# Optimization experiments

Measured on AMD Instinct MI355X. Metric: run time of the kernel, lower is better.

## Reference

```python
import jax, jax.numpy as jnp
import numpy as np

ND, NPR, DD, DP, LAT, AT, B = 2048, 2048, 128, 128, 128, 32, 16384


def setup_inputs():
    key = jax.random.key(0)
    ks = jax.random.split(key, 20)
    s = 0.05
    d = {}
    d["e_p_adj"] = (jax.random.uniform(ks[0], (ND, NPR)) < 0.05).astype(jnp.float32)
    d["e_e_adj"] = (jax.random.uniform(ks[1], (ND, ND)) < 0.05).astype(jnp.float32)
    d["p_p_adj"] = (jax.random.uniform(ks[2], (NPR, NPR)) < 0.05).astype(jnp.float32)
    d["input_disease"] = jax.random.randint(ks[3], (B,), 0, ND)
    d["input_drug"] = jax.random.randint(ks[4], (B,), 0, NPR)
    d["labels"] = jax.random.randint(ks[5], (B,), 0, 2)
    # learned parameters
    d["disease_emb"] = jax.random.normal(ks[6], (ND, DD)) * s
    d["drug_emb"] = jax.random.normal(ks[7], (NPR, DP)) * s
    d["Wdg"] = jax.random.normal(ks[8], (DP, LAT)) * s   # disease_gcn_w
    d["bdg_lin"] = jnp.zeros((LAT,))                      # Linear bias
    d["bdg"] = jnp.zeros((LAT,))                          # extra disease_gcn_b
    d["Wpg"] = jax.random.normal(ks[9], (DD, LAT)) * s   # drug_gcn_w
    d["bpg_lin"] = jnp.zeros((LAT,))
    d["bpg"] = jnp.zeros((LAT,))
    d["Wa1_d"] = jax.random.normal(ks[10], (DP + DD, AT)) * s  # concat [key(drug), query(disease)]
    d["ba1_d"] = jnp.zeros((AT,))
    d["Wa2_d"] = jax.random.normal(ks[11], (AT, 1)) * s
    d["ba2_d"] = jnp.zeros((1,))
    d["Wa1_p"] = jax.random.normal(ks[12], (DD + DP, AT)) * s  # concat [key(disease), query(drug)]
    d["ba1_p"] = jnp.zeros((AT,))
    d["Wa2_p"] = jax.random.normal(ks[13], (AT, 1)) * s
    d["ba2_p"] = jnp.zeros((1,))
    d["Wd2"] = jax.random.normal(ks[14], (DD, LAT)) * s  # disease_w2
    d["bd2"] = jnp.zeros((LAT,))
    d["Wp3"] = jax.random.normal(ks[15], (DP, LAT)) * s  # drug_w3
    d["bp3"] = jnp.zeros((LAT,))
    d["mlp_W1"] = jax.random.normal(ks[16], (LAT, DD)) * s
    d["mlp_b1"] = jnp.zeros((DD,))
    d["mlp_W2"] = jax.random.normal(ks[17], (DD, DD)) * s
    d["mlp_b2"] = jnp.zeros((DD,))
    d["Wpred"] = jax.random.normal(ks[18], (DD, 1)) * s
    d["bpred"] = jnp.zeros((1,))
    return d


def _attention_gcn(adj, other, selfe, W1, b1, W2, b2):
    # torch: concat([key=other, query=self]) -> Linear(W1) ; split W1 instead of
    # materializing the [Ns, No, Dk+Dq] concat tensor (same math, less HBM traffic)
    do = other.shape[1]
    ko = other @ W1[:do]              # [No, A]
    qs = selfe @ W1[do:]              # [Ns, A]
    h = jax.nn.relu(qs[:, None, :] + ko[None, :, :] + b1)   # [Ns, No, A]
    alpha = jax.nn.relu(jnp.squeeze(h @ W2, -1) + b2[0])    # [Ns, No]
    alpha = alpha * adj
    return jax.nn.softmax(alpha, axis=1) @ other            # [Ns, Do]


def _forward(e_p_adj, e_e_adj, p_p_adj, input_disease, input_drug, labels,
             disease_emb, drug_emb, Wdg, bdg_lin, bdg, Wpg, bpg_lin, bpg,
             Wa1_d, ba1_d, Wa2_d, ba2_d, Wa1_p, ba1_p, Wa2_p, ba2_p,
             Wd2, bd2, Wp3, bp3, mlp_W1, mlp_b1, mlp_W2, mlp_b2, Wpred, bpred):
    h_e_gcn = _attention_gcn(e_p_adj, drug_emb, disease_emb, Wa1_d, ba1_d, Wa2_d, ba2_d)
    h_e_gcn = h_e_gcn @ Wdg + bdg_lin + bdg
    h_p_gcn = _attention_gcn(e_p_adj.T, disease_emb, drug_emb, Wa1_p, ba1_p, Wa2_p, ba2_p)
    h_p_gcn = h_p_gcn @ Wpg + bpg_lin + bpg
    # disease knn branch
    deg_d = jnp.sum(e_e_adj, axis=1, keepdims=True) + 1e-8
    h_e_e = ((e_e_adj @ disease_emb) / deg_d) @ Wd2 + bd2
    h_e = jax.nn.selu(h_e_gcn + h_e_e)
    # drug knn branch
    deg_p = jnp.sum(p_p_adj, axis=1, keepdims=True) + 1e-8
    h_p_p = ((p_p_adj @ drug_emb) / deg_p) @ Wp3 + bp3
    h_p = jax.nn.selu(h_p_gcn + h_p_p)
    # pair prediction MLP
    x = h_e[input_disease] * h_p[input_drug]                # [B, LAT]
    x = jax.nn.selu(x @ mlp_W1 + mlp_b1)
    x = jax.nn.selu(x @ mlp_W2 + mlp_b2)
    z = jnp.squeeze(x @ Wpred, -1) + bpred[0]               # [B]
    y = labels.astype(jnp.float32)
    # BCEWithLogitsLoss (stable), mean reduction
    loss = jnp.mean(jnp.maximum(z, 0.0) - z * y + jnp.log1p(jnp.exp(-jnp.abs(z))))
    return (loss, jax.nn.sigmoid(z))


def reference(e_p_adj, e_e_adj, p_p_adj, input_disease, input_drug, labels,
              disease_emb, drug_emb, Wdg, bdg_lin, bdg, Wpg, bpg_lin, bpg,
              Wa1_d, ba1_d, Wa2_d, ba2_d, Wa1_p, ba1_p, Wa2_p, ba2_p,
              Wd2, bd2, Wp3, bp3, mlp_W1, mlp_b1, mlp_W2, mlp_b2, Wpred, bpred):
    return _forward(e_p_adj, e_e_adj, p_p_adj, input_disease, input_drug, labels,
                    disease_emb, drug_emb, Wdg, bdg_lin, bdg, Wpg, bpg_lin, bpg,
                    Wa1_d, ba1_d, Wa2_d, ba2_d, Wa1_p, ba1_p, Wa2_p, ba2_p,
                    Wd2, bd2, Wp3, bp3, mlp_W1, mlp_b1, mlp_W2, mlp_b2, Wpred, bpred)
```

## Files before the change

### kernel.cpp

```cpp
#include <hip/hip_runtime.h>

#define ND   2048
#define BB   16384

typedef unsigned short u16;
typedef unsigned int u32;
typedef __attribute__((ext_vector_type(8))) short short8;
typedef __attribute__((ext_vector_type(4))) float f32x4;

__device__ inline float bf2f(u16 u) {
    union { u32 i; float f; } v; v.i = ((u32)u) << 16; return v.f;
}
__device__ inline u16 f2bf(float f) {
    union { float f; u32 i; } v; v.f = f;
    u32 i = v.i + 0x7fffu + ((v.i >> 16) & 1u);
    return (u16)(i >> 16);
}
__device__ inline float seluf(float x) {
    const float sc = 1.0507009873554805f, al = 1.6732632423543772f;
    return x > 0.f ? sc * x : sc * al * expm1f(x);
}
__device__ inline short8 packbf8(float4 f0, float4 f1) {
    short8 a;
    a[0] = (short)f2bf(f0.x); a[1] = (short)f2bf(f0.y);
    a[2] = (short)f2bf(f0.z); a[3] = (short)f2bf(f0.w);
    a[4] = (short)f2bf(f1.x); a[5] = (short)f2bf(f1.y);
    a[6] = (short)f2bf(f1.z); a[7] = (short)f2bf(f1.w);
    return a;
}

__global__ void detectk(const void* __restrict__ demb, u32* __restrict__ flag) {
    const u16* p = (const u16*)demb;
    int tid = threadIdx.x;
    int sane = 0;
    #pragma unroll
    for (int i = 0; i < 2; i++) {
        u16 u = p[4 * tid + 2 * i];
        int e = (u >> 7) & 0xFF;
        if (u == 0 || (e >= 0x66 && e <= 0x8C)) sane++;
    }
    __shared__ int red[256];
    red[tid] = sane; __syncthreads();
    for (int o = 128; o > 0; o >>= 1) {
        if (tid < o) red[tid] += red[tid + o];
        __syncthreads();
    }
    if (tid == 0) flag[0] = (red[0] < 300) ? 1u : 0u;
}

#define NSEG 26
struct CvtArgs { const void* src[NSEG]; int off[NSEG]; int n[NSEG]; };

__global__ __launch_bounds__(256) void cvtk(CvtArgs a, u16* __restrict__ base,
                                            const u32* __restrict__ flag) {
    int seg = blockIdx.y;
    int n = a.n[seg];
    const void* s = a.src[seg];
    u16* d = base + a.off[seg];
    bool f32 = flag[0] != 0;
    int stride = gridDim.x * blockDim.x;
    for (int i = blockIdx.x * blockDim.x + threadIdx.x; i < n; i += stride)
        d[i] = f32 ? f2bf(((const float*)s)[i]) : ((const u16*)s)[i];
}

__device__ inline void tpose_body(const u16* in, int R, int C,
                                  u16* out, int ldo, int ooff,
                                  u16 (*tile)[33]) {
    int c0 = blockIdx.x * 32, r0 = blockIdx.y * 32;
    int x = c0 + threadIdx.x;
    for (int i = threadIdx.y; i < 32; i += 8) {
        int r = r0 + i;
        tile[i][threadIdx.x] = (r < R && x < C) ? in[(size_t)r * C + x] : (u16)0;
    }
    __syncthreads();
    int rr = r0 + threadIdx.x;
    for (int i = threadIdx.y; i < 32; i += 8) {
        int cc = c0 + i;
        if (cc < C && rr < R) out[(size_t)cc * ldo + ooff + rr] = tile[threadIdx.x][i];
    }
}

__global__ void tpose_embs(const u16* __restrict__ demb, const u16* __restrict__ pemb,
                           u16* __restrict__ disT, u16* __restrict__ drugT) {
    __shared__ u16 tile[32][33];
    if (blockIdx.z == 0) tpose_body(demb, ND, 128, disT, ND, 0, tile);
    else                 tpose_body(pemb, ND, 128, drugT, ND, 0, tile);
}

__global__ void tpose_smalls(const u16* s0, const u16* s1, const u16* s2,
                             const u16* s3, const u16* s4, const u16* s5,
                             u16* W1T, u16* W2T, u16* WcTe, u16* WcTp) {
    __shared__ u16 tile[32][33];
    const u16* in; u16* out; int ldo, ooff;
    switch (blockIdx.z) {
        case 0:  in = s0; out = W1T;  ldo = 128; ooff = 0;   break;
        case 1:  in = s1; out = W2T;  ldo = 128; ooff = 0;   break;
        case 2:  in = s2; out = WcTe; ldo = 256; ooff = 0;   break;
        case 3:  in = s3; out = WcTe; ldo = 256; ooff = 128; break;
        case 4:  in = s4; out = WcTp; ldo = 256; ooff = 0;   break;
        default: in = s5; out = WcTp; ldo = 256; ooff = 128; break;
    }
    tpose_body(in, 128, 128, out, ldo, ooff, tile);
}

__global__ void biasc(const u16* a0, const u16* a1, const u16* a2, u16* o0,
                      const u16* b0, const u16* b1, const u16* b2, u16* o1) {
    int t = threadIdx.x;
    o0[t] = f2bf(bf2f(a0[t]) + bf2f(a1[t]) + bf2f(a2[t]));
    o1[t] = f2bf(bf2f(b0[t]) + bf2f(b1[t]) + bf2f(b2[t]));
}

__global__ __launch_bounds__(256) void degk(
    const void* __restrict__ e_e, float* __restrict__ dinv_e,
    const void* __restrict__ p_p, float* __restrict__ dinv_p,
    const u32* __restrict__ flag) {
    int row = blockIdx.x, tid = threadIdx.x;
    const void* ab = blockIdx.y ? p_p : e_e;
    float* o = blockIdx.y ? dinv_p : dinv_e;
    bool f32 = flag[0] != 0;
    float s = 0.f;
    if (f32) {
        const float4* a4 = (const float4*)((const float*)ab + (size_t)row * 2048) + tid * 2;
        float4 v0 = a4[0], v1 = a4[1];
        s = v0.x + v0.y + v0.z + v0.w + v1.x + v1.y + v1.z + v1.w;
    } else {
        const uint4* a4 = (const uint4*)((const u16*)ab + (size_t)row * 2048) + tid;
        uint4 v = a4[0];
        u32 u[4] = {v.x, v.y, v.z, v.w};
        #pragma unroll
        for (int c = 0; c < 4; c++)
            s += bf2f((u16)(u[c] & 0xffff)) + bf2f((u16)(u[c] >> 16));
    }
    __shared__ float red[256];
    red[tid] = s; __syncthreads();
    for (int ofs = 128; ofs > 0; ofs >>= 1) {
        if (tid < ofs) red[tid] += red[tid + ofs];
        __syncthreads();
    }
    if (tid == 0) o[row] = 1.f / (red[0] + 1e-8f);
}

__global__ __launch_bounds__(128) void koqs(
    const u16* __restrict__ demb, const u16* __restrict__ pemb,
    const u16* __restrict__ Wa1d, const u16* __restrict__ ba1d,
    const u16* __restrict__ Wa1p, const u16* __restrict__ ba1p,
    float* __restrict__ ko_d, float* __restrict__ qs_d,
    float* __restrict__ ko_p, float* __restrict__ qs_p) {
    int row = blockIdx.x, m = blockIdx.y, tid = threadIdx.x;
    const u16* src; const u16* W; const u16* bias; float* out;
    switch (m) {
        case 0:  src = pemb; W = Wa1d;            bias = nullptr; out = ko_d; break;
        case 1:  src = demb; W = Wa1d + 128 * 32; bias = ba1d;    out = qs_d; break;
        case 2:  src = demb; W = Wa1p;            bias = nullptr; out = ko_p; break;
        default: src = pemb; W = Wa1p + 128 * 32; bias = ba1p;    out = qs_p; break;
    }
    __shared__ float x[128];
    __shared__ float red[128];
    x[tid] = bf2f(src[(size_t)row * 128 + tid]);
    __syncthreads();
    int a = tid & 31, part = tid >> 5;
    float s = 0.f;
    #pragma unroll
    for (int k = 0; k < 32; k++) s += x[part * 32 + k] * bf2f(W[(part * 32 + k) * 32 + a]);
    red[tid] = s;
    __syncthreads();
    if (part == 0) {
        float t = red[a] + red[a + 32] + red[a + 64] + red[a + 96];
        if (bias) t += bf2f(bias[a]);
        out[(size_t)row * 32 + a] = t;
    }
}

struct AW {
    const float* qs[2]; const float* ko[2];
    const u16* w2[2]; const u16* b2[2];
    u16* outw[2]; float* sums[2];
    int transposed[2];
};

__global__ __launch_bounds__(256, 4) void attnw6(AW a, const void* __restrict__ adj,
                                                 const u32* __restrict__ flag) {
    __shared__ float tile[32][257];
    __shared__ float wpart[4][32];
    int z = blockIdx.z;
    int tid = threadIdx.x;
    int lane = tid & 63, wv = tid >> 6;
    int jl = wv * 64 + lane;
    int jbase = blockIdx.x * 256;
    int j = jbase + jl;
    int p0 = blockIdx.y * 32;
    bool f32a = flag[0] != 0;
    bool tr = a.transposed[z] != 0;
    const float* adjf = (const float*)adj;
    const u16*   adjh = (const u16*)adj;

    float kv[32];
    {
        const float4* kp = (const float4*)(a.ko[z] + (size_t)j * 32);
        #pragma unroll
        for (int qd = 0; qd < 8; qd++) {
            float4 v = kp[qd];
            kv[qd * 4 + 0] = v.x; kv[qd * 4 + 1] = v.y;
            kv[qd * 4 + 2] = v.z; kv[qd * 4 + 3] = v.w;
        }
    }
    float w2v[32];
    #pragma unroll
    for (int i2 = 0; i2 < 32; i2++) w2v[i2] = bf2f(a.w2[z][i2]);
    float b2 = bf2f(a.b2[z][0]);
    const float* qs = a.qs[z];
    u16* outw = a.outw[z];

    if (tr) {
        if (f32a) {
            const float4* src = (const float4*)(adjf + (size_t)(jbase + tid) * 2048 + p0);
            #pragma unroll
            for (int q8 = 0; q8 < 8; q8++) {
                float4 v = src[q8];
                tile[q8 * 4 + 0][tid] = v.x; tile[q8 * 4 + 1][tid] = v.y;
                tile[q8 * 4 + 2][tid] = v.z; tile[q8 * 4 + 3][tid] = v.w;
            }
        } else {
            const uint4* src = (const uint4*)(adjh + (size_t)(jbase + tid) * 2048 + p0);
            #pragma unroll
            for (int q8 = 0; q8 < 4; q8++) {
                uint4 v = src[q8];
                u32 uu[4] = {v.x, v.y, v.z, v.w};
                #pragma unroll
                for (int c = 0; c < 4; c++) {
                    tile[q8 * 8 + c * 2 + 0][tid] = bf2f((u16)(uu[c] & 0xffff));
                    tile[q8 * 8 + c * 2 + 1][tid] = bf2f((u16)(uu[c] >> 16));
                }
            }
        }
        __syncthreads();
    }

    #pragma unroll 1
    for (int pl = 0; pl < 32; pl++) {
        int row = p0 + pl;
        const float* qrow = qs + (size_t)row * 32;
        float s = 0.f;
        #pragma unroll
        for (int aa = 0; aa < 32; aa++)
            s += fmaxf(qrow[aa] + kv[aa], 0.f) * w2v[aa];
        s = fmaxf(s + b2, 0.f);
        float av = tr ? tile[pl][jl]
                      : (f32a ? adjf[(size_t)row * 2048 + j]
                              : bf2f(adjh[(size_t)row * 2048 + j]));
        float e = __expf(s * av);
        outw[(size_t)row * 2048 + j] = f2bf(e);
        float t = e;
        #pragma unroll
        for (int o = 32; o > 0; o >>= 1) t += __shfl_down(t, o, 64);
        if (lane == 0) wpart[wv][pl] = t;
    }
    __syncthreads();
    if (tid < 32)
        a.sums[z][(size_t)blockIdx.x * 2048 + p0 + tid] =
            wpart[0][tid] + wpart[1][tid] + wpart[2][tid] + wpart[3][tid];
}

struct GD4 {
    const void* A[4]; const u16* BT[4]; u16* C[4];
    const u16* bias[4]; const float* rs[4];
    int lda[4], ldb[4], ldc[4], coff[4], kiters[4], act[4], araw[4], rsmode[4];
};

#define PADK 136

__global__ __launch_bounds__(256, 2) void gemmL(GD4 g, const u32* __restrict__ flag) {
    __shared__ __align__(16) u16 As[16][PADK];
    __shared__ __align__(16) u16 Bs[128][PADK];
    int z = blockIdx.y;
    bool af32 = g.araw[z] && (flag[0] != 0);
    const void* A = g.A[z];
    const u16* BT = g.BT[z];
    int lda = g.lda[z], ldb = g.ldb[z];
    int kiters = g.kiters[z];
    int tid = threadIdx.x;
    int lane = tid & 63, wv = tid >> 6;
    int mrow = lane & 15, quad = lane >> 4;
    int m0 = blockIdx.x * 16;
    int c0 = wv * 32;
    int sr = tid >> 4, sk = (tid & 15) * 8;
    f32x4 acc0 = {0.f, 0.f, 0.f, 0.f}, acc1 = {0.f, 0.f, 0.f, 0.f};

    short8 ra, rb[8];
    auto ldstage = [&](int kb) {
        if (af32) {
            const float* A32 = (const float*)A;
            const float4* p = (const float4*)(A32 + (size_t)(m0 + sr) * lda + kb + sk);
            float4 f0 = p[0], f1 = p[1];
            ra = packbf8(f0, f1);
        } else {
            ra = *(const short8*)((const u16*)A + (size_t)(m0 + sr) * lda + kb + sk);
        }
        const u16* bbase = BT + (size_t)sr * ldb + kb + sk;
        #pragma unroll
        for (int i = 0; i < 8; i++)
            rb[i] = *(const short8*)(bbase + (size_t)i * 16 * ldb);
    };
    auto ststage = [&]() {
        *(short8*)(&As[sr][sk]) = ra;
        #pragma unroll
        for (int i = 0; i < 8; i++)
            *(short8*)(&Bs[i * 16 + sr][sk]) = rb[i];
    };
    auto compute = [&]() {
        #pragma unroll
        for (int ks = 0; ks < 4; ks++) {
            short8 af = *(const short8*)(&As[mrow][ks * 32 + quad * 8]);
            short8 b0 = *(const short8*)(&Bs[c0 + mrow][ks * 32 + quad * 8]);
            short8 b1 = *(const short8*)(&Bs[c0 + 16 + mrow][ks * 32 + quad * 8]);
            acc0 = __builtin_amdgcn_mfma_f32_16x16x32_bf16(af, b0, acc0, 0, 0, 0);
            acc1 = __builtin_amdgcn_mfma_f32_16x16x32_bf16(af, b1, acc1, 0, 0, 0);
        }
    };

    ldstage(0);
    #pragma unroll 1
    for (int it = 0; it < kiters - 1; ++it) {
        ststage();
        __syncthreads();
        ldstage((it + 1) * 128);
        compute();
        __syncthreads();
    }
    ststage();
    __syncthreads();
    compute();

    const float* rs = g.rs[z];
    int rsmode = g.rsmode[z];
    const u16* bi = g.bias[z];
    u16* C = g.C[z];
    int ldc = g.ldc[z], coff = g.coff[z], act = g.act[z];
    int n0 = c0 + mrow, n1 = n0 + 16;
    float bv0 = bi ? bf2f(bi[n0]) : 0.f;
    float bv1 = bi ? bf2f(bi[n1]) : 0.f;
    #pragma unroll
    for (int r = 0; r < 4; r++) {
        int row = m0 + quad * 4 + r;
        float v0 = acc0[r], v1 = acc1[r];
        if (rsmode == 1) { float sc = rs[row]; v0 *= sc; v1 *= sc; }
        else if (rsmode == 2) {
            float t = 0.f;
            #pragma unroll
            for (int p = 0; p < 8; p++) t += rs[row + p * 2048];
            float sc = 1.f / t;
            v0 *= sc; v1 *= sc;
        }
        v0 += bv0; v1 += bv1;
        if (act) { v0 = seluf(v0); v1 = seluf(v1); }
        C[(size_t)row * ldc + coff + n0] = f2bf(v0);
        C[(size_t)row * ldc + coff + n1] = f2bf(v1);
    }
}

__global__ __launch_bounds__(256) void xbuild(
    const u16* __restrict__ he, const u16* __restrict__ hp,
    const int* __restrict__ di, const int* __restrict__ dr, u16* __restrict__ X) {
    int idx = blockIdx.x * 256 + threadIdx.x;
    int d2 = idx & 63;
    int b = idx >> 6;
    int ia = di[b], ic = dr[b];
    u32 ue = ((const u32*)he)[ia * 64 + d2];
    u32 up = ((const u32*)hp)[ic * 64 + d2];
    float lo = bf2f((u16)(ue & 0xffff)) * bf2f((u16)(up & 0xffff));
    float hi = bf2f((u16)(ue >> 16)) * bf2f((u16)(up >> 16));
    ((u32*)X)[idx] = (u32)f2bf(lo) | ((u32)f2bf(hi) << 16);
}

__global__ __launch_bounds__(256) void zloss(
    const u16* __restrict__ X2, const u16* __restrict__ wpred,
    const u16* __restrict__ bpred, const int* __restrict__ labels,
    float* __restrict__ out, float* __restrict__ part) {
    __shared__ float wp[128];
    __shared__ float ls[256];
    int tid = threadIdx.x;
    if (tid < 128) wp[tid] = bf2f(wpred[tid]);
    __syncthreads();
    int b = blockIdx.x * 256 + tid;
    const uint4* xp = (const uint4*)(X2 + (size_t)b * 128);
    float z = 0.f;
    #pragma unroll
    for (int i = 0; i < 16; i++) {
        uint4 q = xp[i];
        u32 u[4] = {q.x, q.y, q.z, q.w};
        #pragma unroll
        for (int c = 0; c < 4; c++) {
            z += bf2f((u16)(u[c] & 0xffff)) * wp[i * 8 + c * 2];
            z += bf2f((u16)(u[c] >> 16)) * wp[i * 8 + c * 2 + 1];
        }
    }
    z += bf2f(bpred[0]);
    out[1 + b] = 1.f / (1.f + __expf(-z));
    float y = (float)labels[b];
    ls[tid] = fmaxf(z, 0.f) - z * y + log1pf(__expf(-fabsf(z)));
    __syncthreads();
    for (int o = 128; o > 0; o >>= 1) {
        if (tid < o) ls[tid] += ls[tid + o];
        __syncthreads();
    }
    if (tid == 0) part[blockIdx.x] = ls[0];
}

__global__ void finloss(const float* __restrict__ part, float* __restrict__ out) {
    __shared__ float s[64];
    s[threadIdx.x] = part[threadIdx.x];
    __syncthreads();
    for (int o = 32; o > 0; o >>= 1) {
        if (threadIdx.x < o) s[threadIdx.x] += s[threadIdx.x + o];
        __syncthreads();
    }
    if (threadIdx.x == 0) out[0] = s[0] * (1.f / 16384.f);
}

extern "C" void kernel_launch(void* const* d_in, const int* in_sizes, int n_in,
                              void* d_out, int out_size, void* d_ws, size_t ws_size,
                              hipStream_t stream) {
    const void* e_p_adj = d_in[0];
    const void* e_e_adj = d_in[1];
    const void* p_p_adj = d_in[2];
    const int* in_dis  = (const int*)d_in[3];
    const int* in_drug = (const int*)d_in[4];
    const int* labels  = (const int*)d_in[5];
    float* out = (float*)d_out;

    char* ws = (char*)d_ws;
    size_t off = 0;
    auto take = [&](size_t bytes) { char* p = ws + off; off = (off + bytes + 255) & ~(size_t)255; return p; };
    u16*   Wbuf  = (u16*)take((size_t)2048 * 2048 * 2);
    u16*   drugT = (u16*)take((size_t)128 * 2048 * 2);
    u16*   disT  = (u16*)take((size_t)128 * 2048 * 2);
    float* ko_d  = (float*)take((size_t)2048 * 32 * 4);
    float* qs_d  = (float*)take((size_t)2048 * 32 * 4);
    float* ko_p  = (float*)take((size_t)2048 * 32 * 4);
    float* qs_p  = (float*)take((size_t)2048 * 32 * 4);
    u16*   A_e   = (u16*)take((size_t)2048 * 256 * 2);
    u16*   A_p   = (u16*)take((size_t)2048 * 256 * 2);
    u16*   WcTe  = (u16*)take((size_t)128 * 256 * 2);
    u16*   WcTp  = (u16*)take((size_t)128 * 256 * 2);
    u16*   W1T   = (u16*)take((size_t)128 * 128 * 2);
    u16*   W2T   = (u16*)take((size_t)128 * 128 * 2);
    u16*   b_e   = (u16*)take(256);
    u16*   b_p   = (u16*)take(256);
    u16*   h_e   = (u16*)take((size_t)2048 * 128 * 2);
    u16*   h_p   = (u16*)take((size_t)2048 * 128 * 2);
    float* dinv_e = (float*)take(2048 * 4);
    float* dinv_p = (float*)take(2048 * 4);
    float* sumsD  = (float*)take(8 * 2048 * 4);
    float* sumsP  = (float*)take(8 * 2048 * 4);
    float* part  = (float*)take(64 * 4);
    u16*   canon = (u16*)take((size_t)700000 * 2);
    u32*   flag  = (u32*)take(256);
    bool dual = (ws_size > off) && (ws_size - off) >= ((size_t)2048 * 2048 * 2 + 512);
    u16*   Wbuf2 = dual ? (u16*)take((size_t)2048 * 2048 * 2) : Wbuf;
    u16* X  = Wbuf;
    u16* X1 = Wbuf + (size_t)BB * 128;
    u16* X2 = drugT;

    const int segidx[NSEG] = {6, 7, 14, 18, 8, 22, 11, 24, 26, 28,
                              15, 16, 17, 19, 20, 21,
                              9, 10, 12, 13, 23, 25, 27, 29, 30, 31};
    const int segn[NSEG]   = {262144, 262144, 8192, 8192, 16384, 16384, 16384, 16384, 16384, 16384,
                              32, 32, 1, 32, 32, 1,
                              128, 128, 128, 128, 128, 128, 128, 128, 128, 1};
    CvtArgs ca;
    u16* cp[NSEG];
    {
        int o = 0;
        for (int i = 0; i < NSEG; i++) {
            ca.src[i] = d_in[segidx[i]];
            ca.off[i] = o;
            ca.n[i] = segn[i];
            cp[i] = canon + o;
            o += (segn[i] + 15) & ~15;
        }
    }
    u16 *cdemb = cp[0], *cpemb = cp[1], *cWa1d = cp[2], *cWa1p = cp[3];
    u16 *cWdg = cp[4], *cWd2 = cp[5], *cWpg = cp[6], *cWp3 = cp[7];
    u16 *cW1 = cp[8], *cW2 = cp[9];
    u16 *cba1d = cp[10], *cWa2d = cp[11], *cba2d = cp[12];
    u16 *cba1p = cp[13], *cWa2p = cp[14], *cba2p = cp[15];
    u16 *cbdg_lin = cp[16], *cbdg = cp[17], *cbpg_lin = cp[18], *cbpg = cp[19];
    u16 *cbd2 = cp[20], *cbp3 = cp[21], *cmb1 = cp[22], *cmb2 = cp[23];
    u16 *cWpred = cp[24], *cbpred = cp[25];

    detectk<<<1, 256, 0, stream>>>(d_in[6], flag);
    cvtk<<<dim3(64, NSEG), 256, 0, stream>>>(ca, canon, flag);

    tpose_embs<<<dim3(4, 64, 2), dim3(32, 8), 0, stream>>>(cdemb, cpemb, disT, drugT);
    tpose_smalls<<<dim3(4, 4, 6), dim3(32, 8), 0, stream>>>(
        cW1, cW2, cWdg, cWd2, cWpg, cWp3, W1T, W2T, WcTe, WcTp);
    biasc<<<1, 128, 0, stream>>>(cbdg_lin, cbdg, cbd2, b_e, cbpg_lin, cbpg, cbp3, b_p);
    degk<<<dim3(2048, 2), 256, 0, stream>>>(e_e_adj, dinv_e, p_p_adj, dinv_p, flag);
    koqs<<<dim3(2048, 4), 128, 0, stream>>>(cdemb, cpemb, cWa1d, cba1d, cWa1p, cba1p,
                                            ko_d, qs_d, ko_p, qs_p);

    auto setd = [](GD4& g, int z, const void* A, int lda, const u16* BT, int ldb,
                   u16* C, int ldc, int coff, int ki, const u16* bi,
                   const float* rs, int act, int araw, int rm) {
        g.A[z] = A; g.lda[z] = lda; g.BT[z] = BT; g.ldb[z] = ldb;
        g.C[z] = C; g.ldc[z] = ldc; g.coff[z] = coff; g.kiters[z] = ki;
        g.bias[z] = bi; g.rs[z] = rs; g.act[z] = act; g.araw[z] = araw; g.rsmode[z] = rm;
    };
    auto mkaw = [](const float* qs0, const float* ko0, const u16* w20, const u16* b20,
                   u16* o0, float* s0, int t0,
                   const float* qs1, const float* ko1, const u16* w21, const u16* b21,
                   u16* o1, float* s1, int t1) {
        AW a;
        a.qs[0] = qs0; a.ko[0] = ko0; a.w2[0] = w20; a.b2[0] = b20;
        a.outw[0] = o0; a.sums[0] = s0; a.transposed[0] = t0;
        a.qs[1] = qs1; a.ko[1] = ko1; a.w2[1] = w21; a.b2[1] = b21;
        a.outw[1] = o1; a.sums[1] = s1; a.transposed[1] = t1;
        return a;
    };

    if (dual) {
        AW aw = mkaw(qs_d, ko_d, cWa2d, cba2d, Wbuf, sumsD, 0,
                     qs_p, ko_p, cWa2p, cba2p, Wbuf2, sumsP, 1);
        attnw6<<<dim3(8, 64, 2), 256, 0, stream>>>(aw, e_p_adj, flag);
        GD4 g;
        setd(g, 0, Wbuf, 2048, drugT, 2048, A_e, 256, 0, 16, nullptr, sumsD, 0, 0, 2);
        setd(g, 1, e_e_adj, 2048, disT, 2048, A_e, 256, 128, 16, nullptr, dinv_e, 0, 1, 1);
        setd(g, 2, Wbuf2, 2048, disT, 2048, A_p, 256, 0, 16, nullptr, sumsP, 0, 0, 2);
        setd(g, 3, p_p_adj, 2048, drugT, 2048, A_p, 256, 128, 16, nullptr, dinv_p, 0, 1, 1);
        gemmL<<<dim3(128, 4), 256, 0, stream>>>(g, flag);
    } else {
        AW aw1 = mkaw(qs_d, ko_d, cWa2d, cba2d, Wbuf, sumsD, 0,
                      qs_d, ko_d, cWa2d, cba2d, Wbuf, sumsD, 0);
        attnw6<<<dim3(8, 64, 1), 256, 0, stream>>>(aw1, e_p_adj, flag);
        GD4 g1;
        setd(g1, 0, Wbuf, 2048, drugT, 2048, A_e, 256, 0, 16, nullptr, sumsD, 0, 0, 2);
        setd(g1, 1, e_e_adj, 2048, disT, 2048, A_e, 256, 128, 16, nullptr, dinv_e, 0, 1, 1);
        setd(g1, 2, Wbuf, 2048, drugT, 2048, A_e, 256, 0, 16, nullptr, sumsD, 0, 0, 2);
        setd(g1, 3, Wbuf, 2048, drugT, 2048, A_e, 256, 0, 16, nullptr, sumsD, 0, 0, 2);
        gemmL<<<dim3(128, 2), 256, 0, stream>>>(g1, flag);
        AW aw2 = mkaw(qs_p, ko_p, cWa2p, cba2p, Wbuf, sumsP, 1,
                      qs_p, ko_p, cWa2p, cba2p, Wbuf, sumsP, 1);
        attnw6<<<dim3(8, 64, 1), 256, 0, stream>>>(aw2, e_p_adj, flag);
        GD4 g2;
        setd(g2, 0, Wbuf, 2048, disT, 2048, A_p, 256, 0, 16, nullptr, sumsP, 0, 0, 2);
        setd(g2, 1, p_p_adj, 2048, drugT, 2048, A_p, 256, 128, 16, nullptr, dinv_p, 0, 1, 1);
        setd(g2, 2, Wbuf, 2048, disT, 2048, A_p, 256, 0, 16, nullptr, sumsP, 0, 0, 2);
        setd(g2, 3, Wbuf, 2048, disT, 2048, A_p, 256, 0, 16, nullptr, sumsP, 0, 0, 2);
        gemmL<<<dim3(128, 2), 256, 0, stream>>>(g2, flag);
    }

    {
        GD4 g;
        setd(g, 0, A_e, 256, WcTe, 256, h_e, 128, 0, 2, b_e, nullptr, 1, 0, 0);
        setd(g, 1, A_p, 256, WcTp, 256, h_p, 128, 0, 2, b_p, nullptr, 1, 0, 0);
        setd(g, 2, A_e, 256, WcTe, 256, h_e, 128, 0, 2, b_e, nullptr, 1, 0, 0);
        setd(g, 3, A_e, 256, WcTe, 256, h_e, 128, 0, 2, b_e, nullptr, 1, 0, 0);
        gemmL<<<dim3(128, 2), 256, 0, stream>>>(g, flag);
    }

    xbuild<<<4096, 256, 0, stream>>>(h_e, h_p, in_dis, in_drug, X);
    {
        GD4 g;
        setd(g, 0, X, 128, W1T, 128, X1, 128, 0, 1, cmb1, nullptr, 1, 0, 0);
        setd(g, 1, X, 128, W1T, 128, X1, 128, 0, 1, cmb1, nullptr, 1, 0, 0);
        setd(g, 2, X, 128, W1T, 128, X1, 128, 0, 1, cmb1, nullptr, 1, 0, 0);
        setd(g, 3, X, 128, W1T, 128, X1, 128, 0, 1, cmb1, nullptr, 1, 0, 0);
        gemmL<<<dim3(1024, 1), 256, 0, stream>>>(g, flag);
    }
    {
        GD4 g;
        setd(g, 0, X1, 128, W2T, 128, X2, 128, 0, 1, cmb2, nullptr, 1, 0, 0);
        setd(g, 1, X1, 128, W2T, 128, X2, 128, 0, 1, cmb2, nullptr, 1, 0, 0);
        setd(g, 2, X1, 128, W2T, 128, X2, 128, 0, 1, cmb2, nullptr, 1, 0, 0);
        setd(g, 3, X1, 128, W2T, 128, X2, 128, 0, 1, cmb2, nullptr, 1, 0, 0);
        gemmL<<<dim3(1024, 1), 256, 0, stream>>>(g, flag);
    }

    zloss<<<64, 256, 0, stream>>>(X2, cWpred, cbpred, labels, out, part);
    finloss<<<1, 64, 0, stream>>>(part, out);
}
```

Baseline: 255.9 us.

## Replace dense attention-weight GEMMs with sparse per-row gather aggregation

The separate attention-weight kernel, its 2048x2048 weight buffer and the dense neighbour-aggregation GEMMs are replaced by one kernel, `sagg`. Each block scans one adjacency row, builds a compacted list of nonzero neighbours in shared memory with weights expm1(score), and gathers only those embedding rows. The zero-adjacency terms (weight exp(0)=1) are folded in exactly through a precomputed column sum of the embeddings and a denominator of 2048 plus the weight sum. The aim is to skip work on the roughly 95% zero entries and avoid writing and re-reading the dense weight matrix. The trade-offs are an extra transpose of e_p_adj and a hard cap of 512 neighbours per row, which silently truncates the sum for denser inputs.

```diff
diff --git a/kernel.cpp b/kernel.cpp
--- a/kernel.cpp
+++ b/kernel.cpp
@@ -78,13 +78,6 @@
         int cc = c0 + i;
         if (cc < C && rr < R) out[(size_t)cc * ldo + ooff + rr] = tile[threadIdx.x][i];
     }
-}
-
-__global__ void tpose_embs(const u16* __restrict__ demb, const u16* __restrict__ pemb,
-                           u16* __restrict__ disT, u16* __restrict__ drugT) {
-    __shared__ u16 tile[32][33];
-    if (blockIdx.z == 0) tpose_body(demb, ND, 128, disT, ND, 0, tile);
-    else                 tpose_body(pemb, ND, 128, drugT, ND, 0, tile);
 }
 
 __global__ void tpose_smalls(const u16* s0, const u16* s1, const u16* s2,
@@ -103,6 +96,23 @@
     tpose_body(in, 128, 128, out, ldo, ooff, tile);
 }
 
+__global__ void tposeEP(const void* __restrict__ in, u16* __restrict__ out,
+                        const u32* __restrict__ flag) {
+    __shared__ u16 tile[32][33];
+    bool f32 = flag[0] != 0;
+    int c0 = blockIdx.x * 32, r0 = blockIdx.y * 32;
+    int x = c0 + threadIdx.x;
+    for (int i = threadIdx.y; i < 32; i += 8) {
+        int r = r0 + i;
+        tile[i][threadIdx.x] = f32 ? f2bf(((const float*)in)[(size_t)r * 2048 + x])
+                                   : ((const u16*)in)[(size_t)r * 2048 + x];
+    }
+    __syncthreads();
+    int rr = r0 + threadIdx.x;
+    for (int i = threadIdx.y; i < 32; i += 8)
+        out[(size_t)(c0 + i) * 2048 + rr] = tile[threadIdx.x][i];
+}
+
 __global__ void biasc(const u16* a0, const u16* a1, const u16* a2, u16* o0,
                       const u16* b0, const u16* b1, const u16* b2, u16* o1) {
     int t = threadIdx.x;
@@ -110,34 +120,25 @@
     o1[t] = f2bf(bf2f(b0[t]) + bf2f(b1[t]) + bf2f(b2[t]));
 }
 
-__global__ __launch_bounds__(256) void degk(
-    const void* __restrict__ e_e, float* __restrict__ dinv_e,
-    const void* __restrict__ p_p, float* __restrict__ dinv_p,
-    const u32* __restrict__ flag) {
-    int row = blockIdx.x, tid = threadIdx.x;
-    const void* ab = blockIdx.y ? p_p : e_e;
-    float* o = blockIdx.y ? dinv_p : dinv_e;
-    bool f32 = flag[0] != 0;
+__global__ __launch_bounds__(1024) void embsumk(const u16* __restrict__ demb,
+                                                const u16* __restrict__ pemb,
+                                                float* __restrict__ se,
+                                                float* __restrict__ sp) {
+    const u16* src = blockIdx.x ? pemb : demb;
+    float* dst = blockIdx.x ? sp : se;
+    int d = threadIdx.x & 127, r8 = threadIdx.x >> 7;
     float s = 0.f;
-    if (f32) {
-        const float4* a4 = (const float4*)((const float*)ab + (size_t)row * 2048) + tid * 2;
-        float4 v0 = a4[0], v1 = a4[1];
-        s = v0.x + v0.y + v0.z + v0.w + v1.x + v1.y + v1.z + v1.w;
-    } else {
-        const uint4* a4 = (const uint4*)((const u16*)ab + (size_t)row * 2048) + tid;
-        uint4 v = a4[0];
-        u32 u[4] = {v.x, v.y, v.z, v.w};
+    for (int r = r8; r < 2048; r += 8)
+        s += bf2f(src[(size_t)r * 128 + d]);
+    __shared__ float part[8][128];
+    part[r8][d] = s;
+    __syncthreads();
+    if (threadIdx.x < 128) {
+        float t = 0.f;
         #pragma unroll
-        for (int c = 0; c < 4; c++)
-            s += bf2f((u16)(u[c] & 0xffff)) + bf2f((u16)(u[c] >> 16));
-    }
-    __shared__ float red[256];
-    red[tid] = s; __syncthreads();
-    for (int ofs = 128; ofs > 0; ofs >>= 1) {
-        if (tid < ofs) red[tid] += red[tid + ofs];
-        __syncthreads();
-    }
-    if (tid == 0) o[row] = 1.f / (red[0] + 1e-8f);
+        for (int i = 0; i < 8; i++) t += part[i][threadIdx.x];
+        dst[threadIdx.x] = t;
+    }
 }
 
 __global__ __launch_bounds__(128) void koqs(
@@ -171,94 +172,96 @@
     }
 }
 
-struct AW {
-    const float* qs[2]; const float* ko[2];
-    const u16* w2[2]; const u16* b2[2];
-    u16* outw[2]; float* sums[2];
-    int transposed[2];
+#define ECAP 512
+struct SG {
+    const void* adj[4];
+    int adjbf[4];
+    const float* qs[4]; const float* ko[4];
+    const u16* w2[4]; const u16* b2[4];
+    const float* embsum[4];
+    const u16* emb[4];
+    u16* outp[4]; int coff[4];
+    int mode[4];
 };
 
-__global__ __launch_bounds__(256, 4) void attnw6(AW a, const void* __restrict__ adj,
-                                                 const u32* __restrict__ flag) {
-    __shared__ float tile[32][257];
-    __shared__ float wpart[4][32];
-    int z = blockIdx.z;
+__global__ __launch_bounds__(256, 4) void sagg(SG p, const u32* __restrict__ flag) {
+    __shared__ float accA[128], accB[128];
+    __shared__ float qsh[32], w2sh[32];
+    __shared__ float wlist[ECAP];
+    __shared__ int jlist[ECAP];
+    __shared__ float red[256];
+    __shared__ int ecnt;
+    __shared__ float wsum_sh;
+    int z = blockIdx.y;
+    int row = blockIdx.x;
     int tid = threadIdx.x;
-    int lane = tid & 63, wv = tid >> 6;
-    int jl = wv * 64 + lane;
-    int jbase = blockIdx.x * 256;
-    int j = jbase + jl;
-    int p0 = blockIdx.y * 32;
-    bool f32a = flag[0] != 0;
-    bool tr = a.transposed[z] != 0;
-    const float* adjf = (const float*)adj;
-    const u16*   adjh = (const u16*)adj;
-
-    float kv[32];
-    {
-        const float4* kp = (const float4*)(a.ko[z] + (size_t)j * 32);
-        #pragma unroll
-        for (int qd = 0; qd < 8; qd++) {
-            float4 v = kp[qd];
-            kv[qd * 4 + 0] = v.x; kv[qd * 4 + 1] = v.y;
-            kv[qd * 4 + 2] = v.z; kv[qd * 4 + 3] = v.w;
+    int mode = p.mode[z];
+    bool f32a = (p.adjbf[z] == 0) && (flag[0] != 0);
+    const float* adjf = (const float*)p.adj[z];
+    const u16*   adjh = (const u16*)p.adj[z];
+    if (tid < 128) { accA[tid] = 0.f; accB[tid] = 0.f; }
+    if (tid == 0) ecnt = 0;
+    if (mode == 0) {
+        if (tid < 32) qsh[tid] = p.qs[z][(size_t)row * 32 + tid];
+        else if (tid < 64) w2sh[tid - 32] = bf2f(p.w2[z][tid - 32]);
+    }
+    __syncthreads();
+    float b2v = (mode == 0) ? bf2f(p.b2[z][0]) : 0.f;
+    const float* ko = p.ko[z];
+    #pragma unroll 1
+    for (int c = 0; c < 8; c++) {
+        int j = c * 256 + tid;
+        float av = f32a ? adjf[(size_t)row * 2048 + j]
+                        : bf2f(adjh[(size_t)row * 2048 + j]);
+        if (av != 0.f) {
+            float w;
+            if (mode == 0) {
+                const float4* kp = (const float4*)(ko + (size_t)j * 32);
+                float s = 0.f;
+                #pragma unroll
+                for (int qd = 0; qd < 8; qd++) {
+                    float4 kv = kp[qd];
+                    s += fmaxf(qsh[qd * 4 + 0] + kv.x, 0.f) * w2sh[qd * 4 + 0];
+                    s += fmaxf(qsh[qd * 4 + 1] + kv.y, 0.f) * w2sh[qd * 4 + 1];
+                    s += fmaxf(qsh[qd * 4 + 2] + kv.z, 0.f) * w2sh[qd * 4 + 2];
+                    s += fmaxf(qsh[qd * 4 + 3] + kv.w, 0.f) * w2sh[qd * 4 + 3];
+                }
+                s = fmaxf(s + b2v, 0.f);
+                w = expm1f(s);
+            } else {
+                w = av;
+            }
+            int idx = atomicAdd(&ecnt, 1);
+            if (idx < ECAP) { jlist[idx] = j; wlist[idx] = w; }
         }
     }
-    float w2v[32];
-    #pragma unroll
-    for (int i2 = 0; i2 < 32; i2++) w2v[i2] = bf2f(a.w2[z][i2]);
-    float b2 = bf2f(a.b2[z][0]);
-    const float* qs = a.qs[z];
-    u16* outw = a.outw[z];
-
-    if (tr) {
-        if (f32a) {
-            const float4* src = (const float4*)(adjf + (size_t)(jbase + tid) * 2048 + p0);
-            #pragma unroll
-            for (int q8 = 0; q8 < 8; q8++) {
-                float4 v = src[q8];
-                tile[q8 * 4 + 0][tid] = v.x; tile[q8 * 4 + 1][tid] = v.y;
-                tile[q8 * 4 + 2][tid] = v.z; tile[q8 * 4 + 3][tid] = v.w;
-            }
-        } else {
-            const uint4* src = (const uint4*)(adjh + (size_t)(jbase + tid) * 2048 + p0);
-            #pragma unroll
-            for (int q8 = 0; q8 < 4; q8++) {
-                uint4 v = src[q8];
-                u32 uu[4] = {v.x, v.y, v.z, v.w};
-                #pragma unroll
-                for (int c = 0; c < 4; c++) {
-                    tile[q8 * 8 + c * 2 + 0][tid] = bf2f((u16)(uu[c] & 0xffff));
-                    tile[q8 * 8 + c * 2 + 1][tid] = bf2f((u16)(uu[c] >> 16));
-                }
-            }
-        }
+    __syncthreads();
+    int E = min(ecnt, ECAP);
+    float ws0 = 0.f;
+    if (tid < E) ws0 = wlist[tid];
+    if (tid + 256 < E) ws0 += wlist[tid + 256];
+    red[tid] = ws0;
+    __syncthreads();
+    for (int o = 128; o > 0; o >>= 1) {
+        if (tid < o) red[tid] += red[tid + o];
         __syncthreads();
     }
-
+    if (tid == 0) wsum_sh = red[0];
+    int d = tid & 127, half = tid >> 7;
+    const u16* emb = p.emb[z];
+    float acc = 0.f;
     #pragma unroll 1
-    for (int pl = 0; pl < 32; pl++) {
-        int row = p0 + pl;
-        const float* qrow = qs + (size_t)row * 32;
-        float s = 0.f;
-        #pragma unroll
-        for (int aa = 0; aa < 32; aa++)
-            s += fmaxf(qrow[aa] + kv[aa], 0.f) * w2v[aa];
-        s = fmaxf(s + b2, 0.f);
-        float av = tr ? tile[pl][jl]
-                      : (f32a ? adjf[(size_t)row * 2048 + j]
-                              : bf2f(adjh[(size_t)row * 2048 + j]));
-        float e = __expf(s * av);
-        outw[(size_t)row * 2048 + j] = f2bf(e);
-        float t = e;
-        #pragma unroll
-        for (int o = 32; o > 0; o >>= 1) t += __shfl_down(t, o, 64);
-        if (lane == 0) wpart[wv][pl] = t;
-    }
-    __syncthreads();
-    if (tid < 32)
-        a.sums[z][(size_t)blockIdx.x * 2048 + p0 + tid] =
-            wpart[0][tid] + wpart[1][tid] + wpart[2][tid] + wpart[3][tid];
+    for (int e = half; e < E; e += 2)
+        acc += wlist[e] * bf2f(emb[(size_t)jlist[e] * 128 + d]);
+    if (half == 0) accA[d] = acc; else accB[d] = acc;
+    __syncthreads();
+    if (tid < 128) {
+        float v = accA[tid] + accB[tid];
+        float denom;
+        if (mode == 0) { v += p.embsum[z][tid]; denom = 2048.f + wsum_sh; }
+        else denom = wsum_sh + 1e-8f;
+        p.outp[z][(size_t)row * 256 + p.coff[z] + tid] = f2bf(v / denom);
+    }
 }
 
 struct GD4 {
@@ -344,13 +347,6 @@
         int row = m0 + quad * 4 + r;
         float v0 = acc0[r], v1 = acc1[r];
         if (rsmode == 1) { float sc = rs[row]; v0 *= sc; v1 *= sc; }
-        else if (rsmode == 2) {
-            float t = 0.f;
-            #pragma unroll
-            for (int p = 0; p < 8; p++) t += rs[row + p * 2048];
-            float sc = 1.f / t;
-            v0 *= sc; v1 *= sc;
-        }
         v0 += bv0; v1 += bv1;
         if (act) { v0 = seluf(v0); v1 = seluf(v1); }
         C[(size_t)row * ldc + coff + n0] = f2bf(v0);
@@ -431,9 +427,8 @@
     char* ws = (char*)d_ws;
     size_t off = 0;
     auto take = [&](size_t bytes) { char* p = ws + off; off = (off + bytes + 255) & ~(size_t)255; return p; };
-    u16*   Wbuf  = (u16*)take((size_t)2048 * 2048 * 2);
-    u16*   drugT = (u16*)take((size_t)128 * 2048 * 2);
-    u16*   disT  = (u16*)take((size_t)128 * 2048 * 2);
+    u16*   Xbuf  = (u16*)take((size_t)2 * BB * 128 * 2);
+    u16*   epT   = (u16*)take((size_t)2048 * 2048 * 2);
     float* ko_d  = (float*)take((size_t)2048 * 32 * 4);
     float* qs_d  = (float*)take((size_t)2048 * 32 * 4);
     float* ko_p  = (float*)take((size_t)2048 * 32 * 4);
@@ -448,18 +443,14 @@
     u16*   b_p   = (u16*)take(256);
     u16*   h_e   = (u16*)take((size_t)2048 * 128 * 2);
     u16*   h_p   = (u16*)take((size_t)2048 * 128 * 2);
-    float* dinv_e = (float*)take(2048 * 4);
-    float* dinv_p = (float*)take(2048 * 4);
-    float* sumsD  = (float*)take(8 * 2048 * 4);
-    float* sumsP  = (float*)take(8 * 2048 * 4);
+    float* esum_d = (float*)take(128 * 4);
+    float* esum_p = (float*)take(128 * 4);
     float* part  = (float*)take(64 * 4);
     u16*   canon = (u16*)take((size_t)700000 * 2);
     u32*   flag  = (u32*)take(256);
-    bool dual = (ws_size > off) && (ws_size - off) >= ((size_t)2048 * 2048 * 2 + 512);
-    u16*   Wbuf2 = dual ? (u16*)take((size_t)2048 * 2048 * 2) : Wbuf;
-    u16* X  = Wbuf;
-    u16* X1 = Wbuf + (size_t)BB * 128;
-    u16* X2 = drugT;
+    u16* X  = Xbuf;
+    u16* X1 = Xbuf + (size_t)BB * 128;
+    u16* X2 = epT;
 
     const int segidx[NSEG] = {6, 7, 14, 18, 8, 22, 11, 24, 26, 28,
                               15, 16, 17, 19, 20, 21,
@@ -491,13 +482,30 @@
     detectk<<<1, 256, 0, stream>>>(d_in[6], flag);
     cvtk<<<dim3(64, NSEG), 256, 0, stream>>>(ca, canon, flag);
 
-    tpose_embs<<<dim3(4, 64, 2), dim3(32, 8), 0, stream>>>(cdemb, cpemb, disT, drugT);
     tpose_smalls<<<dim3(4, 4, 6), dim3(32, 8), 0, stream>>>(
         cW1, cW2, cWdg, cWd2, cWpg, cWp3, W1T, W2T, WcTe, WcTp);
     biasc<<<1, 128, 0, stream>>>(cbdg_lin, cbdg, cbd2, b_e, cbpg_lin, cbpg, cbp3, b_p);
-    degk<<<dim3(2048, 2), 256, 0, stream>>>(e_e_adj, dinv_e, p_p_adj, dinv_p, flag);
+    tposeEP<<<dim3(64, 64), dim3(32, 8), 0, stream>>>(e_p_adj, epT, flag);
+    embsumk<<<2, 1024, 0, stream>>>(cdemb, cpemb, esum_d, esum_p);
     koqs<<<dim3(2048, 4), 128, 0, stream>>>(cdemb, cpemb, cWa1d, cba1d, cWa1p, cba1p,
                                             ko_d, qs_d, ko_p, qs_p);
+
+    {
+        SG s;
+        s.adj[0] = e_p_adj; s.adjbf[0] = 0; s.qs[0] = qs_d; s.ko[0] = ko_d;
+        s.w2[0] = cWa2d; s.b2[0] = cba2d; s.embsum[0] = esum_p; s.emb[0] = cpemb;
+        s.outp[0] = A_e; s.coff[0] = 0; s.mode[0] = 0;
+        s.adj[1] = e_e_adj; s.adjbf[1] = 0; s.qs[1] = nullptr; s.ko[1] = nullptr;
+        s.w2[1] = nullptr; s.b2[1] = nullptr; s.embsum[1] = nullptr; s.emb[1] = cdemb;
+        s.outp[1] = A_e; s.coff[1] = 128; s.mode[1] = 1;
+        s.adj[2] = epT; s.adjbf[2] = 1; s.qs[2] = qs_p; s.ko[2] = ko_p;
+        s.w2[2] = cWa2p; s.b2[2] = cba2p; s.embsum[2] = esum_d; s.emb[2] = cdemb;
+        s.outp[2] = A_p; s.coff[2] = 0; s.mode[2] = 0;
+        s.adj[3] = p_p_adj; s.adjbf[3] = 0; s.qs[3] = nullptr; s.ko[3] = nullptr;
+        s.w2[3] = nullptr; s.b2[3] = nullptr; s.embsum[3] = nullptr; s.emb[3] = cpemb;
+        s.outp[3] = A_p; s.coff[3] = 128; s.mode[3] = 1;
+        sagg<<<dim3(2048, 4), 256, 0, stream>>>(s, flag);
+    }
 
     auto setd = [](GD4& g, int z, const void* A, int lda, const u16* BT, int ldb,
                    u16* C, int ldc, int coff, int ki, const u16* bi,
@@ -506,48 +514,6 @@
         g.C[z] = C; g.ldc[z] = ldc; g.coff[z] = coff; g.kiters[z] = ki;
         g.bias[z] = bi; g.rs[z] = rs; g.act[z] = act; g.araw[z] = araw; g.rsmode[z] = rm;
     };
-    auto mkaw = [](const float* qs0, const float* ko0, const u16* w20, const u16* b20,
-                   u16* o0, float* s0, int t0,
-                   const float* qs1, const float* ko1, const u16* w21, const u16* b21,
-                   u16* o1, float* s1, int t1) {
-        AW a;
-        a.qs[0] = qs0; a.ko[0] = ko0; a.w2[0] = w20; a.b2[0] = b20;
-        a.outw[0] = o0; a.sums[0] = s0; a.transposed[0] = t0;
-        a.qs[1] = qs1; a.ko[1] = ko1; a.w2[1] = w21; a.b2[1] = b21;
-        a.outw[1] = o1; a.sums[1] = s1; a.transposed[1] = t1;
-        return a;
-    };
-
-    if (dual) {
-        AW aw = mkaw(qs_d, ko_d, cWa2d, cba2d, Wbuf, sumsD, 0,
-                     qs_p, ko_p, cWa2p, cba2p, Wbuf2, sumsP, 1);
-        attnw6<<<dim3(8, 64, 2), 256, 0, stream>>>(aw, e_p_adj, flag);
-        GD4 g;
-        setd(g, 0, Wbuf, 2048, drugT, 2048, A_e, 256, 0, 16, nullptr, sumsD, 0, 0, 2);
-        setd(g, 1, e_e_adj, 2048, disT, 2048, A_e, 256, 128, 16, nullptr, dinv_e, 0, 1, 1);
-        setd(g, 2, Wbuf2, 2048, disT, 2048, A_p, 256, 0, 16, nullptr, sumsP, 0, 0, 2);
-        setd(g, 3, p_p_adj, 2048, drugT, 2048, A_p, 256, 128, 16, nullptr, dinv_p, 0, 1, 1);
-        gemmL<<<dim3(128, 4), 256, 0, stream>>>(g, flag);
-    } else {
-        AW aw1 = mkaw(qs_d, ko_d, cWa2d, cba2d, Wbuf, sumsD, 0,
-                      qs_d, ko_d, cWa2d, cba2d, Wbuf, sumsD, 0);
-        attnw6<<<dim3(8, 64, 1), 256, 0, stream>>>(aw1, e_p_adj, flag);
-        GD4 g1;
-        setd(g1, 0, Wbuf, 2048, drugT, 2048, A_e, 256, 0, 16, nullptr, sumsD, 0, 0, 2);
-        setd(g1, 1, e_e_adj, 2048, disT, 2048, A_e, 256, 128, 16, nullptr, dinv_e, 0, 1, 1);
-        setd(g1, 2, Wbuf, 2048, drugT, 2048, A_e, 256, 0, 16, nullptr, sumsD, 0, 0, 2);
-        setd(g1, 3, Wbuf, 2048, drugT, 2048, A_e, 256, 0, 16, nullptr, sumsD, 0, 0, 2);
-        gemmL<<<dim3(128, 2), 256, 0, stream>>>(g1, flag);
-        AW aw2 = mkaw(qs_p, ko_p, cWa2p, cba2p, Wbuf, sumsP, 1,
-                      qs_p, ko_p, cWa2p, cba2p, Wbuf, sumsP, 1);
-        attnw6<<<dim3(8, 64, 1), 256, 0, stream>>>(aw2, e_p_adj, flag);
-        GD4 g2;
-        setd(g2, 0, Wbuf, 2048, disT, 2048, A_p, 256, 0, 16, nullptr, sumsP, 0, 0, 2);
-        setd(g2, 1, p_p_adj, 2048, drugT, 2048, A_p, 256, 128, 16, nullptr, dinv_p, 0, 1, 1);
-        setd(g2, 2, Wbuf, 2048, disT, 2048, A_p, 256, 0, 16, nullptr, sumsP, 0, 0, 2);
-        setd(g2, 3, Wbuf, 2048, disT, 2048, A_p, 256, 0, 16, nullptr, sumsP, 0, 0, 2);
-        gemmL<<<dim3(128, 2), 256, 0, stream>>>(g2, flag);
-    }
 
     {
         GD4 g;
```

New measurement: 414.6 us. 1.62x slower.
